# Performance work log

Hardware: AMD Instinct MI355X
Metric: run time of the kernel (lower is better)

Reference implementation:

```python
import jax, jax.numpy as jnp
import numpy as np

B, H, W, C = 64, 32, 32, 256
HZ, WZ = 16, 16
N = 64          # hidden_dim = n_proposals
K = 3           # dynamic depthwise kernel size
EPS = 1e-5


def _layernorm(x, g, b):
    mu = jnp.mean(x, axis=-1, keepdims=True)
    var = jnp.var(x, axis=-1, keepdims=True)
    return (x - mu) * jax.lax.rsqrt(var + EPS) * g + b


def setup_inputs() -> dict:
    key = jax.random.key(0)
    ks = jax.random.split(key, 8)
    s = 0.02  # weight init scale
    return {
        "x_feat": jax.random.normal(ks[0], (B, H, W, C), jnp.float32),
        "z_feat": jax.random.normal(ks[1], (B, HZ, WZ, C), jnp.float32),
        "Wz": jax.random.normal(ks[2], (C, N), jnp.float32) * s,
        "bz": jnp.zeros((N,), jnp.float32),
        "Wx": jax.random.normal(ks[3], (C, N), jnp.float32) * s,
        "bx": jnp.zeros((N,), jnp.float32),
        "Wdyn": jax.random.normal(ks[4], (C, N + K), jnp.float32) * s,
        "bdyn": jnp.zeros((N + K,), jnp.float32),
        "g_norm": jnp.ones((C,), jnp.float32),
        "b_norm": jnp.zeros((C,), jnp.float32),
        "Wp": jax.random.normal(ks[5], (C, 1), jnp.float32) * s,
        "bp": jnp.zeros((1,), jnp.float32),
        "g_ln": jnp.ones((C,), jnp.float32),
        "b_ln": jnp.zeros((C,), jnp.float32),
    }


def _dysep_conv_atten(query, value, Wdyn, bdyn, g_norm, b_norm):
    # query, value: [B, N, C]
    dy = query @ Wdyn + bdyn                      # [B, N, N+K]
    w_depth = dy[:, :, :K]                        # [B, N, K] per-channel depthwise kernels
    w_point = dy[:, :, K:]                        # [B, N, N] per-sample pointwise (1x1) weights
    # depthwise conv along C with 'same' padding (torch conv1d = cross-correlation)
    vpad = jnp.pad(value, ((0, 0), (0, 0), (1, 1)))
    depth = (w_depth[..., 0:1] * vpad[:, :, 0:C]
             + w_depth[..., 1:2] * vpad[:, :, 1:C + 1]
             + w_depth[..., 2:3] * vpad[:, :, 2:C + 2])
    depth = jax.nn.relu(depth)                    # [B, N, C]
    point = jnp.einsum('bnm,bmc->bnc', w_point, depth)
    return _layernorm(point, g_norm, b_norm)


def reference(x_feat, z_feat, Wz, bz, Wx, bx, Wdyn, bdyn,
              g_norm, b_norm, Wp, bp, g_ln, b_ln):
    # kernels from template features (detached in the original: kernels.detach())
    z_core = z_feat @ Wz + bz                                   # [B,HZ,WZ,N]
    kernels = jnp.einsum('bhwn,bhwc->bnc', z_core, z_feat)      # [B,N,C]
    kernels = jax.lax.stop_gradient(kernels)

    x_n = x_feat @ Wx + bx                                      # [B,H,W,N]
    kernels_x = jnp.einsum('bhwn,bhwc->bnc', x_n, x_feat)       # [B,N,C]
    kernels_x = _dysep_conv_atten(kernels, kernels_x, Wdyn, bdyn, g_norm, b_norm)

    x_corr = jnp.einsum('bnc,bhwn->bhwc', kernels_x, x_n)       # [B,H,W,C]
    proto = kernels_x @ Wp + bp                                 # [B,N,1]
    tem = jax.nn.sigmoid(jnp.einsum('bnd,bnc->bdc', proto, kernels_x))  # [B,1,C]
    tem = tem[:, :, None, :]                                    # [B,1,1,C]
    x_corr = x_corr * tem

    return x_feat + jax.nn.relu(_layernorm(x_corr, g_ln, b_ln))
```

## Files before the change

kernel.cpp:

```cpp
#include <hip/hip_runtime.h>
#include <math.h>

#define EPSV 1e-5f

typedef __attribute__((ext_vector_type(8))) short short8;
typedef __attribute__((ext_vector_type(4))) float f32x4;

static __device__ __forceinline__ unsigned bfpack2(float lo, float hi) {
    union { float f; unsigned u; } a, b;
    a.f = lo; b.f = hi;
    unsigned ua = a.u + 0x7fffu + ((a.u >> 16) & 1u);
    unsigned ub = b.u + 0x7fffu + ((b.u >> 16) & 1u);
    return (ua >> 16) | (ub & 0xffff0000u);
}

__global__ __launch_bounds__(256) void gemm_all(
    const float* __restrict__ Xx, const float* __restrict__ Wxp,
    const float* __restrict__ bxp, float* __restrict__ Yx,
    const float* __restrict__ Xz, const float* __restrict__ Wzp,
    const float* __restrict__ bzp,
    unsigned short* __restrict__ xnbT, unsigned short* __restrict__ xfbT,
    unsigned short* __restrict__ zcbT, unsigned short* __restrict__ zfbT)
{
    __shared__ float Xc[16 * 132];
    __shared__ float Wc[16 * 64];
    const int t = threadIdx.x;
    const float *X, *W, *bias; float* Y;
    unsigned short *Tn, *Tf;
    long r0; int P, bb, p0;
    if (blockIdx.x < 512) {
        X = Xx; W = Wxp; bias = bxp; Y = Yx;
        r0 = (long)blockIdx.x * 128;
        P = 1024; bb = blockIdx.x >> 3; p0 = (blockIdx.x & 7) * 128;
        Tn = xnbT; Tf = xfbT;
    } else {
        int zb = blockIdx.x - 512;
        X = Xz; W = Wzp; bias = bzp; Y = nullptr;
        r0 = (long)zb * 128;
        P = 256; bb = zb >> 1; p0 = (zb & 1) * 128;
        Tn = zcbT; Tf = zfbT;
    }

    const int tr = t >> 4, tc = t & 15;
    float4 bv = *(const float4*)(bias + tc * 4);
    float acc[8][4];
#pragma unroll
    for (int i = 0; i < 8; ++i) { acc[i][0]=bv.x; acc[i][1]=bv.y; acc[i][2]=bv.z; acc[i][3]=bv.w; }

    const int lr = t >> 2;
    const int lc = (t & 3) * 4;
    const int wl = t >> 4, wj = (t & 15) * 4;
    float4 xv0 = *(const float4*)(X + (r0 + lr) * 256 + lc);
    float4 xv1 = *(const float4*)(X + (r0 + lr + 64) * 256 + lc);
    float4 wv  = *(const float4*)(W + (long)wl * 64 + wj);

    for (int c0 = 0; c0 < 256; c0 += 16) {
        Xc[(lc+0)*132 + lr] = xv0.x; Xc[(lc+1)*132 + lr] = xv0.y;
        Xc[(lc+2)*132 + lr] = xv0.z; Xc[(lc+3)*132 + lr] = xv0.w;
        Xc[(lc+0)*132 + lr+64] = xv1.x; Xc[(lc+1)*132 + lr+64] = xv1.y;
        Xc[(lc+2)*132 + lr+64] = xv1.z; Xc[(lc+3)*132 + lr+64] = xv1.w;
        *(float4*)&Wc[wl * 64 + wj] = wv;
        __syncthreads();
        if (c0 + 16 < 256) {
            xv0 = *(const float4*)(X + (r0 + lr) * 256 + c0 + 16 + lc);
            xv1 = *(const float4*)(X + (r0 + lr + 64) * 256 + c0 + 16 + lc);
            wv  = *(const float4*)(W + (long)(c0 + 16 + wl) * 64 + wj);
        }
#pragma unroll
        for (int cl = 0; cl < 16; ++cl) {
            float4 a0 = *(float4*)&Xc[cl * 132 + tr * 8];
            float4 a1 = *(float4*)&Xc[cl * 132 + tr * 8 + 4];
            float4 b4 = *(float4*)&Wc[cl * 64 + tc * 4];
            acc[0][0]+=a0.x*b4.x; acc[0][1]+=a0.x*b4.y; acc[0][2]+=a0.x*b4.z; acc[0][3]+=a0.x*b4.w;
            acc[1][0]+=a0.y*b4.x; acc[1][1]+=a0.y*b4.y; acc[1][2]+=a0.y*b4.z; acc[1][3]+=a0.y*b4.w;
            acc[2][0]+=a0.z*b4.x; acc[2][1]+=a0.z*b4.y; acc[2][2]+=a0.z*b4.z; acc[2][3]+=a0.z*b4.w;
            acc[3][0]+=a0.w*b4.x; acc[3][1]+=a0.w*b4.y; acc[3][2]+=a0.w*b4.z; acc[3][3]+=a0.w*b4.w;
            acc[4][0]+=a1.x*b4.x; acc[4][1]+=a1.x*b4.y; acc[4][2]+=a1.x*b4.z; acc[4][3]+=a1.x*b4.w;
            acc[5][0]+=a1.y*b4.x; acc[5][1]+=a1.y*b4.y; acc[5][2]+=a1.y*b4.z; acc[5][3]+=a1.y*b4.w;
            acc[6][0]+=a1.z*b4.x; acc[6][1]+=a1.z*b4.y; acc[6][2]+=a1.z*b4.z; acc[6][3]+=a1.z*b4.w;
            acc[7][0]+=a1.w*b4.x; acc[7][1]+=a1.w*b4.y; acc[7][2]+=a1.w*b4.z; acc[7][3]+=a1.w*b4.w;
        }
        {
            int cl2 = t >> 4, p8 = (t & 15) * 8;
            const float* xr = &Xc[cl2 * 132 + p8];
            uint4 pk;
            pk.x = bfpack2(xr[0], xr[1]); pk.y = bfpack2(xr[2], xr[3]);
            pk.z = bfpack2(xr[4], xr[5]); pk.w = bfpack2(xr[6], xr[7]);
            *(uint4*)(Tf + ((long)(bb * 256 + c0 + cl2)) * P + p0 + p8) = pk;
        }
        __syncthreads();
    }
    if (Y) {
#pragma unroll
        for (int i = 0; i < 8; ++i) {
            float4 o = make_float4(acc[i][0], acc[i][1], acc[i][2], acc[i][3]);
            *(float4*)(Y + (r0 + tr * 8 + i) * 64 + tc * 4) = o;
        }
    }
#pragma unroll
    for (int j = 0; j < 4; ++j) {
        int n = tc * 4 + j;
        uint4 pk;
        pk.x = bfpack2(acc[0][j], acc[1][j]);
        pk.y = bfpack2(acc[2][j], acc[3][j]);
        pk.z = bfpack2(acc[4][j], acc[5][j]);
        pk.w = bfpack2(acc[6][j], acc[7][j]);
        *(uint4*)(Tn + ((long)(bb * 64 + n)) * P + p0 + tr * 8) = pk;
    }
}

__global__ __launch_bounds__(256) void corr_mfma(
    const unsigned short* __restrict__ xnbT, const unsigned short* __restrict__ xfbT,
    float* __restrict__ kxr,
    const unsigned short* __restrict__ zcbT, const unsigned short* __restrict__ zfbT,
    float* __restrict__ kern)
{
    __shared__ __align__(16) unsigned short AT[64 * 136];
    __shared__ __align__(16) unsigned short BT[64 * 136];
    const int t = threadIdx.x;
    const unsigned short *Ab, *Bb; float* S; int b, P;
    if (blockIdx.y < 64) { b = blockIdx.y;      Ab = xnbT; Bb = xfbT; S = kxr;  P = 1024; }
    else                 { b = blockIdx.y - 64; Ab = zcbT; Bb = zfbT; S = kern; P = 256;  }
    const int ct = blockIdx.x;
    const int w = t >> 6, l = t & 63;
    const int quad = l >> 4, lane16 = l & 15;

    const unsigned short* Abase = Ab + (long)b * 64 * P;
    const unsigned short* Bbase = Bb + ((long)(b * 256 + ct * 64)) * P;
    const int srow = t >> 4, sk = (t & 15) * 8;

    f32x4 acc[4] = {{0.f,0.f,0.f,0.f},{0.f,0.f,0.f,0.f},{0.f,0.f,0.f,0.f},{0.f,0.f,0.f,0.f}};

    uint4 pa[4], pb[4];
#pragma unroll
    for (int i = 0; i < 4; ++i) {
        int row = srow + i * 16;
        pa[i] = *(const uint4*)(Abase + (long)row * P + sk);
        pb[i] = *(const uint4*)(Bbase + (long)row * P + sk);
    }
    const int nk = P >> 7;
    for (int kc = 0; kc < nk; ++kc) {
#pragma unroll
        for (int i = 0; i < 4; ++i) {
            int row = srow + i * 16;
            *(uint4*)&AT[row * 136 + sk] = pa[i];
            *(uint4*)&BT[row * 136 + sk] = pb[i];
        }
        __syncthreads();
        if (kc + 1 < nk) {
            int ko = (kc + 1) * 128 + sk;
#pragma unroll
            for (int i = 0; i < 4; ++i) {
                int row = srow + i * 16;
                pa[i] = *(const uint4*)(Abase + (long)row * P + ko);
                pb[i] = *(const uint4*)(Bbase + (long)row * P + ko);
            }
        }
#pragma unroll
        for (int ks = 0; ks < 4; ++ks) {
            const int ko2 = ks * 32 + quad * 8;
            short8 bfrag = *(const short8*)&BT[(w * 16 + lane16) * 136 + ko2];
#pragma unroll
            for (int mi = 0; mi < 4; ++mi) {
                short8 afrag = *(const short8*)&AT[(mi * 16 + lane16) * 136 + ko2];
                acc[mi] = __builtin_amdgcn_mfma_f32_16x16x32_bf16(afrag, bfrag, acc[mi], 0, 0, 0);
            }
        }
        __syncthreads();
    }
#pragma unroll
    for (int mi = 0; mi < 4; ++mi) {
        long row = (long)(b * 64 + mi * 16 + quad * 4);
        int col = ct * 64 + w * 16 + lane16;
#pragma unroll
        for (int r = 0; r < 4; ++r)
            S[(row + r) * 256 + col] = acc[mi][r];
    }
}

__global__ __launch_bounds__(256) void dy_all(
    const float* __restrict__ kern, const float* __restrict__ Wdyn,
    const float* __restrict__ bdyn, float* __restrict__ dyb)
{
    __shared__ float Ac[16 * 64];
    __shared__ float Wc[16 * 64];
    __shared__ float Wd3[48];
    const int b = blockIdx.x, t = threadIdx.x;
    const int tr = t >> 4, tc = t & 15;
    float acc[4][4];
#pragma unroll
    for (int j = 0; j < 4; ++j) {
        float bj = bdyn[3 + tc * 4 + j];
        acc[0][j] = bj; acc[1][j] = bj; acc[2][j] = bj; acc[3][j] = bj;
    }
    const int lr = t >> 2, lc = (t & 3) * 4;
    const int wl = t >> 4, wj = (t & 15) * 4;
    const int nwd = t / 3, jwd = t - nwd * 3;
    float wdacc = 0.f;
    float4 av = *(const float4*)(kern + ((long)(b * 64 + lr)) * 256 + lc);
    float w0 = Wdyn[wl * 67 + 3 + wj + 0];
    float w1 = Wdyn[wl * 67 + 3 + wj + 1];
    float w2 = Wdyn[wl * 67 + 3 + wj + 2];
    float w3 = Wdyn[wl * 67 + 3 + wj + 3];
    float wdr = (t < 48) ? Wdyn[(t / 3) * 67 + (t % 3)] : 0.f;

    for (int c0 = 0; c0 < 256; c0 += 16) {
        Ac[(lc+0)*64 + lr] = av.x; Ac[(lc+1)*64 + lr] = av.y;
        Ac[(lc+2)*64 + lr] = av.z; Ac[(lc+3)*64 + lr] = av.w;
        Wc[wl*64 + wj+0] = w0; Wc[wl*64 + wj+1] = w1;
        Wc[wl*64 + wj+2] = w2; Wc[wl*64 + wj+3] = w3;
        if (t < 48) Wd3[t] = wdr;
        __syncthreads();
        if (c0 + 16 < 256) {
            av = *(const float4*)(kern + ((long)(b * 64 + lr)) * 256 + c0 + 16 + lc);
            w0 = Wdyn[(c0 + 16 + wl) * 67 + 3 + wj + 0];
            w1 = Wdyn[(c0 + 16 + wl) * 67 + 3 + wj + 1];
            w2 = Wdyn[(c0 + 16 + wl) * 67 + 3 + wj + 2];
            w3 = Wdyn[(c0 + 16 + wl) * 67 + 3 + wj + 3];
            if (t < 48) wdr = Wdyn[(c0 + 16 + t / 3) * 67 + (t % 3)];
        }
#pragma unroll
        for (int cl = 0; cl < 16; ++cl) {
            float4 a = *(float4*)&Ac[cl * 64 + tr * 4];
            float4 w = *(float4*)&Wc[cl * 64 + tc * 4];
            acc[0][0]+=a.x*w.x; acc[0][1]+=a.x*w.y; acc[0][2]+=a.x*w.z; acc[0][3]+=a.x*w.w;
            acc[1][0]+=a.y*w.x; acc[1][1]+=a.y*w.y; acc[1][2]+=a.y*w.z; acc[1][3]+=a.y*w.w;
            acc[2][0]+=a.z*w.x; acc[2][1]+=a.z*w.y; acc[2][2]+=a.z*w.z; acc[2][3]+=a.z*w.w;
            acc[3][0]+=a.w*w.x; acc[3][1]+=a.w*w.y; acc[3][2]+=a.w*w.z; acc[3][3]+=a.w*w.w;
        }
        if (t < 192) {
#pragma unroll
            for (int cl = 0; cl < 16; ++cl)
                wdacc += Ac[cl * 64 + nwd] * Wd3[cl * 3 + jwd];
        }
        __syncthreads();
    }
#pragma unroll
    for (int i = 0; i < 4; ++i) {
        float4 o = make_float4(acc[i][0], acc[i][1], acc[i][2], acc[i][3]);
        *(float4*)(dyb + ((long)(b * 64 + tr * 4 + i)) * 68 + tc * 4) = o;
    }
    if (t < 192) dyb[((long)(b * 64 + nwd)) * 68 + 64 + jwd] = wdacc + bdyn[jwd];
}

__global__ __launch_bounds__(256) void depthpoint(
    const float* __restrict__ dyb, const float* __restrict__ v,
    const float* __restrict__ g, const float* __restrict__ Wp,
    float* __restrict__ point, float* __restrict__ partials)
{
    __shared__ float smem[13312];
    float* wpT = smem;
    float* wd3 = smem + 4352;
    float* vt  = smem + 4608;
    float* dep = smem + 8960;
    float* rs  = vt;

    const int t = threadIdx.x;
    const int b = blockIdx.y, ct = blockIdx.x, c0 = ct * 64;
    const int tr = t >> 4, tc = t & 15;

#pragma unroll
    for (int i = 0; i < 4; ++i) {
        int idx = t + i * 256; int n = idx >> 4, m0 = (idx & 15) * 4;
        float4 w4 = *(const float4*)(dyb + ((long)(b * 64 + n)) * 68 + m0);
        wpT[(m0+0)*68 + n] = w4.x; wpT[(m0+1)*68 + n] = w4.y;
        wpT[(m0+2)*68 + n] = w4.z; wpT[(m0+3)*68 + n] = w4.w;
    }
    if (t < 64) {
        long o = ((long)(b * 64 + t)) * 68 + 64;
        wd3[t*4+0] = dyb[o+0]; wd3[t*4+1] = dyb[o+1]; wd3[t*4+2] = dyb[o+2];
    }
    {
        int m = t >> 2, lc0 = (t & 3) * 17;
#pragma unroll
        for (int k = 0; k < 17; ++k) {
            int lc = lc0 + k;
            if (lc < 66) {
                int c = c0 - 1 + lc;
                vt[m * 68 + lc] = (c >= 0 && c < 256) ? v[((long)(b * 64 + m)) * 256 + c] : 0.f;
            }
        }
    }
    __syncthreads();
#pragma unroll
    for (int im = 0; im < 4; ++im) {
        int m = tr * 4 + im;
        float w0 = wd3[m*4+0], w1 = wd3[m*4+1], w2 = wd3[m*4+2];
#pragma unroll
        for (int jc = 0; jc < 4; ++jc) {
            int cl = tc * 4 + jc;
            float d = w0 * vt[m*68 + cl] + w1 * vt[m*68 + cl + 1] + w2 * vt[m*68 + cl + 2];
            dep[m*68 + cl] = fmaxf(d, 0.f);
        }
    }
    __syncthreads();
    float acc[4][4] = {};
#pragma unroll 16
    for (int m = 0; m < 64; ++m) {
        float4 a4 = *(float4*)&wpT[m * 68 + tr * 4];
        float4 d4 = *(float4*)&dep[m * 68 + tc * 4];
        acc[0][0]+=a4.x*d4.x; acc[0][1]+=a4.x*d4.y; acc[0][2]+=a4.x*d4.z; acc[0][3]+=a4.x*d4.w;
        acc[1][0]+=a4.y*d4.x; acc[1][1]+=a4.y*d4.y; acc[1][2]+=a4.y*d4.z; acc[1][3]+=a4.y*d4.w;
        acc[2][0]+=a4.z*d4.x; acc[2][1]+=a4.z*d4.y; acc[2][2]+=a4.z*d4.z; acc[2][3]+=a4.z*d4.w;
        acc[3][0]+=a4.w*d4.x; acc[3][1]+=a4.w*d4.y; acc[3][2]+=a4.w*d4.z; acc[3][3]+=a4.w*d4.w;
    }
    int cg = c0 + tc * 4;
    float4 g4  = *(const float4*)(g + cg);
    float4 wp4 = *(const float4*)(Wp + cg);
    float gw0 = g4.x*wp4.x, gw1 = g4.y*wp4.y, gw2 = g4.z*wp4.z, gw3 = g4.w*wp4.w;
#pragma unroll
    for (int i = 0; i < 4; ++i) {
        float4 o = make_float4(acc[i][0], acc[i][1], acc[i][2], acc[i][3]);
        *(float4*)(point + ((long)(b * 64 + tr * 4 + i)) * 256 + cg) = o;
        float s  = o.x + o.y + o.z + o.w;
        float s2 = o.x*o.x + o.y*o.y + o.z*o.z + o.w*o.w;
        float dg = o.x*gw0 + o.y*gw1 + o.z*gw2 + o.w*gw3;
        rs[0*1088 + (tr*4+i)*17 + tc] = s;
        rs[1*1088 + (tr*4+i)*17 + tc] = s2;
        rs[2*1088 + (tr*4+i)*17 + tc] = dg;
    }
    __syncthreads();
    if (t < 64) {
        float s = 0.f, s2 = 0.f, dg = 0.f;
#pragma unroll
        for (int j = 0; j < 16; ++j) {
            s  += rs[t*17 + j];
            s2 += rs[1088 + t*17 + j];
            dg += rs[2176 + t*17 + j];
        }
        long base = ((long)(b * 4 + ct)) * 192;
        partials[base + t]        = s;
        partials[base + 64 + t]   = s2;
        partials[base + 128 + t]  = dg;
    }
}

__global__ __launch_bounds__(256) void lntem(
    const float* __restrict__ partials, const float* __restrict__ point,
    const float* __restrict__ g, const float* __restrict__ bta,
    const float* __restrict__ Wp, const float* __restrict__ bp,
    float* __restrict__ murr, float* __restrict__ AB)
{
    __shared__ float sA[256], sB[256];
    __shared__ float wnv[64];
    __shared__ float tot[4];
    const int b = blockIdx.x, t = threadIdx.x;
    const int c = t;
    float gc = g[c], bc = bta[c], wpc = Wp[c];
    sA[t] = gc * wpc; sB[t] = bc * wpc;
    __syncthreads();
    for (int off = 128; off >= 1; off >>= 1) {
        if (t < off) { sA[t] += sA[t+off]; sB[t] += sB[t+off]; }
        __syncthreads();
    }
    if (t == 0) { tot[0] = sA[0]; tot[1] = sB[0] + bp[0]; }
    __syncthreads();
    float Sgw = tot[0], Sbw = tot[1];

    float protoe = 0.f, mu = 0.f, rr = 0.f;
    if (t < 64) {
        float S1 = 0.f, S2 = 0.f, Sdg = 0.f;
#pragma unroll
        for (int ct = 0; ct < 4; ++ct) {
            long o = ((long)(b * 4 + ct)) * 192;
            S1 += partials[o + t]; S2 += partials[o + 64 + t]; Sdg += partials[o + 128 + t];
        }
        mu = S1 * (1.f / 256.f);
        float var = S2 * (1.f / 256.f) - mu * mu;
        rr = rsqrtf(var + EPSV);
        protoe = rr * (Sdg - mu * Sgw) + Sbw;
        wnv[t] = protoe * rr;
        murr[b * 128 + 2*t]     = rr;
        murr[b * 128 + 2*t + 1] = -mu * rr;
    }
    __syncthreads();
    sA[t] = (t < 64) ? protoe * rr * mu : 0.f;
    sB[t] = (t < 64) ? protoe : 0.f;
    __syncthreads();
    for (int off = 128; off >= 1; off >>= 1) {
        if (t < off) { sA[t] += sA[t+off]; sB[t] += sB[t+off]; }
        __syncthreads();
    }
    if (t == 0) { tot[2] = sA[0]; tot[3] = sB[0]; }
    __syncthreads();
    float Bv = tot[2], Sv = tot[3];

    const float* pcol = point + (long)b * 64 * 256 + c;
    float a0 = 0.f, a1 = 0.f, a2 = 0.f, a3 = 0.f;
#pragma unroll
    for (int n = 0; n < 64; n += 4) {
        a0 += wnv[n+0] * pcol[(n+0) * 256];
        a1 += wnv[n+1] * pcol[(n+1) * 256];
        a2 += wnv[n+2] * pcol[(n+2) * 256];
        a3 += wnv[n+3] * pcol[(n+3) * 256];
    }
    float accA = a0 + a1 + a2 + a3;
    float x = gc * (accA - Bv) + bc * Sv;
    float temv = 1.f / (1.f + expf(-x));
    AB[b * 512 + c]       = gc * temv;
    AB[b * 512 + 256 + c] = bc * temv;
}

__global__ __launch_bounds__(256) void final_kernel(
    const float* __restrict__ xn, const float* __restrict__ point,
    const float* __restrict__ murr, const float* __restrict__ AB,
    const float* __restrict__ xf, const float* __restrict__ g,
    const float* __restrict__ bt, float* __restrict__ out)
{
    __shared__ float xtT[64 * 68];
    __shared__ float kc[64 * 68];
    __shared__ float rs1[64 * 17], rs2[64 * 17];
    __shared__ float mu[64], rr[64];
    __shared__ float rq[128];
    const int t = threadIdx.x;
    const int b = blockIdx.y;
    const int pg = blockIdx.x;
    const int tr = t >> 4;
    const int tc = t & 15;

    if (t < 128) rq[t] = murr[b * 128 + t];
    {
        int row = t >> 2, q = t & 3;
        const float* src = xn + ((long)(b * 1024 + pg * 64 + row)) * 64 + q * 16;
        float4 f0 = *(const float4*)(src + 0);
        float4 f1 = *(const float4*)(src + 4);
        float4 f2 = *(const float4*)(src + 8);
        float4 f3 = *(const float4*)(src + 12);
        int n0 = q * 16;
        xtT[(n0+ 0)*68+row]=f0.x; xtT[(n0+ 1)*68+row]=f0.y; xtT[(n0+ 2)*68+row]=f0.z; xtT[(n0+ 3)*68+row]=f0.w;
        xtT[(n0+ 4)*68+row]=f1.x; xtT[(n0+ 5)*68+row]=f1.y; xtT[(n0+ 6)*68+row]=f1.z; xtT[(n0+ 7)*68+row]=f1.w;
        xtT[(n0+ 8)*68+row]=f2.x; xtT[(n0+ 9)*68+row]=f2.y; xtT[(n0+10)*68+row]=f2.z; xtT[(n0+11)*68+row]=f2.w;
        xtT[(n0+12)*68+row]=f3.x; xtT[(n0+13)*68+row]=f3.y; xtT[(n0+14)*68+row]=f3.z; xtT[(n0+15)*68+row]=f3.w;
    }

    float4 xcv[4][4];
    float si[4] = {0.f,0.f,0.f,0.f}, s2i[4] = {0.f,0.f,0.f,0.f};
#pragma unroll
    for (int cc = 0; cc < 4; ++cc) {
        __syncthreads();
#pragma unroll
        for (int i = 0; i < 4; ++i) {
            int idx = t + i * 256;
            int n = idx >> 4, jq = idx & 15;
            int cb = cc * 64 + jq * 4;
            float4 p4 = *(const float4*)(point + ((long)(b * 64 + n)) * 256 + cb);
            float rn = rq[2*n], qn = rq[2*n + 1];
            float4 A4 = *(const float4*)(AB + b * 512 + cb);
            float4 B4 = *(const float4*)(AB + b * 512 + 256 + cb);
            float4 kv;
            kv.x = (p4.x * rn + qn) * A4.x + B4.x;
            kv.y = (p4.y * rn + qn) * A4.y + B4.y;
            kv.z = (p4.z * rn + qn) * A4.z + B4.z;
            kv.w = (p4.w * rn + qn) * A4.w + B4.w;
            *(float4*)&kc[n * 68 + jq * 4] = kv;
        }
        __syncthreads();
        float4 a0 = {0,0,0,0}, a1 = {0,0,0,0}, a2 = {0,0,0,0}, a3 = {0,0,0,0};
#pragma unroll 8
        for (int n = 0; n < 64; ++n) {
            float4 xv = *(float4*)&xtT[n * 68 + tr * 4];
            float4 kv = *(float4*)&kc[n * 68 + tc * 4];
            a0.x += xv.x*kv.x; a0.y += xv.x*kv.y; a0.z += xv.x*kv.z; a0.w += xv.x*kv.w;
            a1.x += xv.y*kv.x; a1.y += xv.y*kv.y; a1.z += xv.y*kv.z; a1.w += xv.y*kv.w;
            a2.x += xv.z*kv.x; a2.y += xv.z*kv.y; a2.z += xv.z*kv.z; a2.w += xv.z*kv.w;
            a3.x += xv.w*kv.x; a3.y += xv.w*kv.y; a3.z += xv.w*kv.z; a3.w += xv.w*kv.w;
        }
        xcv[cc][0] = a0; xcv[cc][1] = a1; xcv[cc][2] = a2; xcv[cc][3] = a3;
        si[0] += a0.x+a0.y+a0.z+a0.w;  s2i[0] += a0.x*a0.x+a0.y*a0.y+a0.z*a0.z+a0.w*a0.w;
        si[1] += a1.x+a1.y+a1.z+a1.w;  s2i[1] += a1.x*a1.x+a1.y*a1.y+a1.z*a1.z+a1.w*a1.w;
        si[2] += a2.x+a2.y+a2.z+a2.w;  s2i[2] += a2.x*a2.x+a2.y*a2.y+a2.z*a2.z+a2.w*a2.w;
        si[3] += a3.x+a3.y+a3.z+a3.w;  s2i[3] += a3.x*a3.x+a3.y*a3.y+a3.z*a3.z+a3.w*a3.w;
    }
#pragma unroll
    for (int i = 0; i < 4; ++i) { rs1[(tr*4+i)*17 + tc] = si[i]; rs2[(tr*4+i)*17 + tc] = s2i[i]; }
    __syncthreads();
    if (t < 64) {
        float s = 0.f, s2 = 0.f;
#pragma unroll
        for (int k = 0; k < 16; ++k) { s += rs1[t*17 + k]; s2 += rs2[t*17 + k]; }
        float m = s * (1.f / 256.f);
        mu[t] = m; rr[t] = rsqrtf(s2 * (1.f / 256.f) - m * m + EPSV);
    }
    __syncthreads();
#pragma unroll
    for (int cc = 0; cc < 4; ++cc) {
        int cb = cc * 64 + tc * 4;
        float4 g4 = *(const float4*)(g + cb);
        float4 b4 = *(const float4*)(bt + cb);
#pragma unroll
        for (int i = 0; i < 4; ++i) {
            int row = tr * 4 + i;
            float m = mu[row], r = rr[row];
            long grow = ((long)(b * 1024 + pg * 64 + row)) * 256;
            float4 xfv = *(const float4*)(xf + grow + cb);
            float4 a = xcv[cc][i];
            float4 o;
            o.x = xfv.x + fmaxf((a.x - m) * r * g4.x + b4.x, 0.f);
            o.y = xfv.y + fmaxf((a.y - m) * r * g4.y + b4.y, 0.f);
            o.z = xfv.z + fmaxf((a.z - m) * r * g4.z + b4.z, 0.f);
            o.w = xfv.w + fmaxf((a.w - m) * r * g4.w + b4.w, 0.f);
            *(float4*)(out + grow + cb) = o;
        }
    }
}

extern "C" void kernel_launch(void* const* d_in, const int* in_sizes, int n_in,
                              void* d_out, int out_size, void* d_ws, size_t ws_size,
                              hipStream_t stream)
{
    (void)in_sizes; (void)n_in; (void)out_size; (void)ws_size;
    const float* x_feat = (const float*)d_in[0];
    const float* z_feat = (const float*)d_in[1];
    const float* Wz     = (const float*)d_in[2];
    const float* bz     = (const float*)d_in[3];
    const float* Wx     = (const float*)d_in[4];
    const float* bx     = (const float*)d_in[5];
    const float* Wdyn   = (const float*)d_in[6];
    const float* bdyn   = (const float*)d_in[7];
    const float* g_norm = (const float*)d_in[8];
    const float* b_norm = (const float*)d_in[9];
    const float* Wp     = (const float*)d_in[10];
    const float* bp     = (const float*)d_in[11];
    const float* g_ln   = (const float*)d_in[12];
    const float* b_ln   = (const float*)d_in[13];
    float* out = (float*)d_out;

    float* ws       = (float*)d_ws;
    float* xn       = ws;
    float* kern     = xn + 4194304;
    float* kxr      = kern + 1048576;
    float* point    = kxr + 1048576;
    float* dyb      = point + 1048576;
    float* partials = dyb + 278528;
    float* murr     = partials + 49152;
    float* AB       = murr + 8192;
    unsigned short* xnbT = (unsigned short*)(AB + 32768);
    unsigned short* xfbT = xnbT + 4194304;
    unsigned short* zcbT = xfbT + 16777216;
    unsigned short* zfbT = zcbT + 1048576;

    gemm_all<<<640, 256, 0, stream>>>(x_feat, Wx, bx, xn, z_feat, Wz, bz,
                                      xnbT, xfbT, zcbT, zfbT);
    corr_mfma<<<dim3(4, 128), 256, 0, stream>>>(xnbT, xfbT, kxr, zcbT, zfbT, kern);
    dy_all<<<64, 256, 0, stream>>>(kern, Wdyn, bdyn, dyb);
    depthpoint<<<dim3(4, 64), 256, 0, stream>>>(dyb, kxr, g_norm, Wp, point, partials);
    lntem<<<64, 256, 0, stream>>>(partials, point, g_norm, b_norm, Wp, bp, murr, AB);
    final_kernel<<<dim3(16, 64), 256, 0, stream>>>(xn, point, murr, AB, x_feat, g_ln, b_ln, out);
}
```

Before: 285.8 us.

## Reassociate projections via per-batch Gram matrices and fold Wx into final GEMM

Replaces the x/z projection GEMM plus correlation with a per-batch Gram matrix X^T X (bf16 MFMA) followed by a small projection by W, with bias handled through column sums. The final stage no longer reads the projected x_n. Instead it builds a per-batch 256x256 matrix M = kernels_x^T-scaled times Wx and runs an MFMA GEMM straight from x_feat, with LayerNorm fused in. This avoids writing and reading the large transposed bf16 copies of x_feat and x_n. In exchange it does more FLOPs on the Gram matrices and reads x_feat with strided column loads, and the reassociation changes bf16 rounding.

```diff
diff --git a/kernel.cpp b/kernel.cpp
--- a/kernel.cpp
+++ b/kernel.cpp
@@ -14,167 +14,155 @@
     return (ua >> 16) | (ub & 0xffff0000u);
 }
 
-__global__ __launch_bounds__(256) void gemm_all(
-    const float* __restrict__ Xx, const float* __restrict__ Wxp,
-    const float* __restrict__ bxp, float* __restrict__ Yx,
-    const float* __restrict__ Xz, const float* __restrict__ Wzp,
-    const float* __restrict__ bzp,
-    unsigned short* __restrict__ xnbT, unsigned short* __restrict__ xfbT,
-    unsigned short* __restrict__ zcbT, unsigned short* __restrict__ zfbT)
-{
-    __shared__ float Xc[16 * 132];
-    __shared__ float Wc[16 * 64];
+__global__ __launch_bounds__(256) void gram(
+    const float* __restrict__ Xx, const float* __restrict__ Xz,
+    float* __restrict__ Gx, float* __restrict__ Gz,
+    float* __restrict__ csx, float* __restrict__ csz)
+{
+    __shared__ __align__(16) unsigned short AT[64 * 72];
+    __shared__ __align__(16) unsigned short BT[64 * 72];
+    __shared__ float csr[256];
+    int id = blockIdx.x;
+    const float* X; float* G; float* cs; int P;
+    if (id < 1024) { X = Xx; G = Gx; cs = csx; P = 1024; }
+    else { id -= 1024; X = Xz; G = Gz; cs = csz; P = 256; }
+    const int b = id & 63;
+    const int tile = id >> 6;
+    const int ci = tile >> 2, cj = tile & 3;
+    const int nk = P >> 6;
     const int t = threadIdx.x;
-    const float *X, *W, *bias; float* Y;
-    unsigned short *Tn, *Tf;
-    long r0; int P, bb, p0;
-    if (blockIdx.x < 512) {
-        X = Xx; W = Wxp; bias = bxp; Y = Yx;
-        r0 = (long)blockIdx.x * 128;
-        P = 1024; bb = blockIdx.x >> 3; p0 = (blockIdx.x & 7) * 128;
-        Tn = xnbT; Tf = xfbT;
-    } else {
-        int zb = blockIdx.x - 512;
-        X = Xz; W = Wzp; bias = bzp; Y = nullptr;
-        r0 = (long)zb * 128;
-        P = 256; bb = zb >> 1; p0 = (zb & 1) * 128;
-        Tn = zcbT; Tf = zfbT;
-    }
-
-    const int tr = t >> 4, tc = t & 15;
-    float4 bv = *(const float4*)(bias + tc * 4);
-    float acc[8][4];
-#pragma unroll
-    for (int i = 0; i < 8; ++i) { acc[i][0]=bv.x; acc[i][1]=bv.y; acc[i][2]=bv.z; acc[i][3]=bv.w; }
-
-    const int lr = t >> 2;
-    const int lc = (t & 3) * 4;
-    const int wl = t >> 4, wj = (t & 15) * 4;
-    float4 xv0 = *(const float4*)(X + (r0 + lr) * 256 + lc);
-    float4 xv1 = *(const float4*)(X + (r0 + lr + 64) * 256 + lc);
-    float4 wv  = *(const float4*)(W + (long)wl * 64 + wj);
-
-    for (int c0 = 0; c0 < 256; c0 += 16) {
-        Xc[(lc+0)*132 + lr] = xv0.x; Xc[(lc+1)*132 + lr] = xv0.y;
-        Xc[(lc+2)*132 + lr] = xv0.z; Xc[(lc+3)*132 + lr] = xv0.w;
-        Xc[(lc+0)*132 + lr+64] = xv1.x; Xc[(lc+1)*132 + lr+64] = xv1.y;
-        Xc[(lc+2)*132 + lr+64] = xv1.z; Xc[(lc+3)*132 + lr+64] = xv1.w;
-        *(float4*)&Wc[wl * 64 + wj] = wv;
-        __syncthreads();
-        if (c0 + 16 < 256) {
-            xv0 = *(const float4*)(X + (r0 + lr) * 256 + c0 + 16 + lc);
-            xv1 = *(const float4*)(X + (r0 + lr + 64) * 256 + c0 + 16 + lc);
-            wv  = *(const float4*)(W + (long)(c0 + 16 + wl) * 64 + wj);
-        }
-#pragma unroll
-        for (int cl = 0; cl < 16; ++cl) {
-            float4 a0 = *(float4*)&Xc[cl * 132 + tr * 8];
-            float4 a1 = *(float4*)&Xc[cl * 132 + tr * 8 + 4];
-            float4 b4 = *(float4*)&Wc[cl * 64 + tc * 4];
-            acc[0][0]+=a0.x*b4.x; acc[0][1]+=a0.x*b4.y; acc[0][2]+=a0.x*b4.z; acc[0][3]+=a0.x*b4.w;
-            acc[1][0]+=a0.y*b4.x; acc[1][1]+=a0.y*b4.y; acc[1][2]+=a0.y*b4.z; acc[1][3]+=a0.y*b4.w;
-            acc[2][0]+=a0.z*b4.x; acc[2][1]+=a0.z*b4.y; acc[2][2]+=a0.z*b4.z; acc[2][3]+=a0.z*b4.w;
-            acc[3][0]+=a0.w*b4.x; acc[3][1]+=a0.w*b4.y; acc[3][2]+=a0.w*b4.z; acc[3][3]+=a0.w*b4.w;
-            acc[4][0]+=a1.x*b4.x; acc[4][1]+=a1.x*b4.y; acc[4][2]+=a1.x*b4.z; acc[4][3]+=a1.x*b4.w;
-            acc[5][0]+=a1.y*b4.x; acc[5][1]+=a1.y*b4.y; acc[5][2]+=a1.y*b4.z; acc[5][3]+=a1.y*b4.w;
-            acc[6][0]+=a1.z*b4.x; acc[6][1]+=a1.z*b4.y; acc[6][2]+=a1.z*b4.z; acc[6][3]+=a1.z*b4.w;
-            acc[7][0]+=a1.w*b4.x; acc[7][1]+=a1.w*b4.y; acc[7][2]+=a1.w*b4.z; acc[7][3]+=a1.w*b4.w;
-        }
-        {
-            int cl2 = t >> 4, p8 = (t & 15) * 8;
-            const float* xr = &Xc[cl2 * 132 + p8];
-            uint4 pk;
-            pk.x = bfpack2(xr[0], xr[1]); pk.y = bfpack2(xr[2], xr[3]);
-            pk.z = bfpack2(xr[4], xr[5]); pk.w = bfpack2(xr[6], xr[7]);
-            *(uint4*)(Tf + ((long)(bb * 256 + c0 + cl2)) * P + p0 + p8) = pk;
-        }
-        __syncthreads();
-    }
-    if (Y) {
-#pragma unroll
-        for (int i = 0; i < 8; ++i) {
-            float4 o = make_float4(acc[i][0], acc[i][1], acc[i][2], acc[i][3]);
-            *(float4*)(Y + (r0 + tr * 8 + i) * 64 + tc * 4) = o;
-        }
-    }
-#pragma unroll
-    for (int j = 0; j < 4; ++j) {
-        int n = tc * 4 + j;
-        uint4 pk;
-        pk.x = bfpack2(acc[0][j], acc[1][j]);
-        pk.y = bfpack2(acc[2][j], acc[3][j]);
-        pk.z = bfpack2(acc[4][j], acc[5][j]);
-        pk.w = bfpack2(acc[6][j], acc[7][j]);
-        *(uint4*)(Tn + ((long)(bb * 64 + n)) * P + p0 + tr * 8) = pk;
-    }
-}
-
-__global__ __launch_bounds__(256) void corr_mfma(
-    const unsigned short* __restrict__ xnbT, const unsigned short* __restrict__ xfbT,
+    const int cl = t & 63, ph = t >> 6;
+    const int w = t >> 6, quad = (t >> 4) & 3, lane16 = t & 15;
+    const float* Xb = X + (long)b * P * 256;
+    const float* Acol = Xb + ci * 64 + cl;
+    const float* Bcol = Xb + cj * 64 + cl;
+    const bool diag = (ci == cj);
+
+    f32x4 acc[4] = {{0.f,0.f,0.f,0.f},{0.f,0.f,0.f,0.f},{0.f,0.f,0.f,0.f},{0.f,0.f,0.f,0.f}};
+    float csum = 0.f;
+
+    for (int kc = 0; kc < nk; ++kc) {
+        const int p0 = kc * 64 + ph * 16;
+        float va[16], vb[16];
+#pragma unroll
+        for (int k = 0; k < 16; ++k) va[k] = Acol[(long)(p0 + k) * 256];
+        if (!diag) {
+#pragma unroll
+            for (int k = 0; k < 16; ++k) vb[k] = Bcol[(long)(p0 + k) * 256];
+        } else {
+#pragma unroll
+            for (int k = 0; k < 16; ++k) { vb[k] = va[k]; csum += va[k]; }
+        }
+        uint4 a0, a1, b0, b1;
+        a0.x = bfpack2(va[0], va[1]);   a0.y = bfpack2(va[2], va[3]);
+        a0.z = bfpack2(va[4], va[5]);   a0.w = bfpack2(va[6], va[7]);
+        a1.x = bfpack2(va[8], va[9]);   a1.y = bfpack2(va[10], va[11]);
+        a1.z = bfpack2(va[12], va[13]); a1.w = bfpack2(va[14], va[15]);
+        b0.x = bfpack2(vb[0], vb[1]);   b0.y = bfpack2(vb[2], vb[3]);
+        b0.z = bfpack2(vb[4], vb[5]);   b0.w = bfpack2(vb[6], vb[7]);
+        b1.x = bfpack2(vb[8], vb[9]);   b1.y = bfpack2(vb[10], vb[11]);
+        b1.z = bfpack2(vb[12], vb[13]); b1.w = bfpack2(vb[14], vb[15]);
+        __syncthreads();
+        *(uint4*)&AT[cl * 72 + ph * 16]     = a0;
+        *(uint4*)&AT[cl * 72 + ph * 16 + 8] = a1;
+        *(uint4*)&BT[cl * 72 + ph * 16]     = b0;
+        *(uint4*)&BT[cl * 72 + ph * 16 + 8] = b1;
+        __syncthreads();
+#pragma unroll
+        for (int ks = 0; ks < 2; ++ks) {
+            const int ko = ks * 32 + quad * 8;
+            short8 bfrag = *(const short8*)&BT[(w * 16 + lane16) * 72 + ko];
+#pragma unroll
+            for (int mi = 0; mi < 4; ++mi) {
+                short8 afrag = *(const short8*)&AT[(mi * 16 + lane16) * 72 + ko];
+                acc[mi] = __builtin_amdgcn_mfma_f32_16x16x32_bf16(afrag, bfrag, acc[mi], 0, 0, 0);
+            }
+        }
+    }
+#pragma unroll
+    for (int mi = 0; mi < 4; ++mi) {
+        long row = (long)(b * 256 + ci * 64 + mi * 16 + quad * 4);
+        int col = cj * 64 + w * 16 + lane16;
+#pragma unroll
+        for (int r = 0; r < 4; ++r)
+            G[(row + r) * 256 + col] = acc[mi][r];
+    }
+    if (diag) {
+        csr[ph * 64 + cl] = csum;
+        __syncthreads();
+        if (t < 64)
+            cs[b * 256 + ci * 64 + t] = csr[t] + csr[64 + t] + csr[128 + t] + csr[192 + t];
+    }
+}
+
+__global__ __launch_bounds__(256) void proj(
+    const float* __restrict__ Gx, const float* __restrict__ csx,
+    const float* __restrict__ Wx, const float* __restrict__ bx,
     float* __restrict__ kxr,
-    const unsigned short* __restrict__ zcbT, const unsigned short* __restrict__ zfbT,
+    const float* __restrict__ Gz, const float* __restrict__ csz,
+    const float* __restrict__ Wz, const float* __restrict__ bz,
     float* __restrict__ kern)
 {
-    __shared__ __align__(16) unsigned short AT[64 * 136];
-    __shared__ __align__(16) unsigned short BT[64 * 136];
+    __shared__ __align__(16) unsigned short ATW[64 * 264];
+    __shared__ __align__(16) unsigned short BTC[64 * 72];
     const int t = threadIdx.x;
-    const unsigned short *Ab, *Bb; float* S; int b, P;
-    if (blockIdx.y < 64) { b = blockIdx.y;      Ab = xnbT; Bb = xfbT; S = kxr;  P = 1024; }
-    else                 { b = blockIdx.y - 64; Ab = zcbT; Bb = zfbT; S = kern; P = 256;  }
-    const int ct = blockIdx.x;
-    const int w = t >> 6, l = t & 63;
-    const int quad = l >> 4, lane16 = l & 15;
-
-    const unsigned short* Abase = Ab + (long)b * 64 * P;
-    const unsigned short* Bbase = Bb + ((long)(b * 256 + ct * 64)) * P;
-    const int srow = t >> 4, sk = (t & 15) * 8;
-
+    const int id = blockIdx.x;
+    const int b = id & 63, s = id >> 6;
+    const float *G, *cs, *W, *bias; float* O;
+    if (s < 4) { G = Gx; cs = csx; W = Wx; bias = bx; O = kxr; }
+    else       { G = Gz; cs = csz; W = Wz; bias = bz; O = kern; }
+    const int ct = s & 3;
+    const int n = t & 63, ph = t >> 6;
+#pragma unroll
+    for (int cc = 0; cc < 4; ++cc) {
+        float v[16];
+#pragma unroll
+        for (int k = 0; k < 16; ++k) v[k] = W[(ph * 64 + cc * 16 + k) * 64 + n];
+        uint4 p0, p1;
+        p0.x = bfpack2(v[0], v[1]);   p0.y = bfpack2(v[2], v[3]);
+        p0.z = bfpack2(v[4], v[5]);   p0.w = bfpack2(v[6], v[7]);
+        p1.x = bfpack2(v[8], v[9]);   p1.y = bfpack2(v[10], v[11]);
+        p1.z = bfpack2(v[12], v[13]); p1.w = bfpack2(v[14], v[15]);
+        *(uint4*)&ATW[n * 264 + ph * 64 + cc * 16]     = p0;
+        *(uint4*)&ATW[n * 264 + ph * 64 + cc * 16 + 8] = p1;
+    }
+    const int row = t >> 2, cq = t & 3;
+    const int w = t >> 6, quad = (t >> 4) & 3, lane16 = t & 15;
+    const float* Grow = G + ((long)(b * 256 + ct * 64 + row)) * 256 + cq * 16;
     f32x4 acc[4] = {{0.f,0.f,0.f,0.f},{0.f,0.f,0.f,0.f},{0.f,0.f,0.f,0.f},{0.f,0.f,0.f,0.f}};
-
-    uint4 pa[4], pb[4];
-#pragma unroll
-    for (int i = 0; i < 4; ++i) {
-        int row = srow + i * 16;
-        pa[i] = *(const uint4*)(Abase + (long)row * P + sk);
-        pb[i] = *(const uint4*)(Bbase + (long)row * P + sk);
-    }
-    const int nk = P >> 7;
-    for (int kc = 0; kc < nk; ++kc) {
-#pragma unroll
-        for (int i = 0; i < 4; ++i) {
-            int row = srow + i * 16;
-            *(uint4*)&AT[row * 136 + sk] = pa[i];
-            *(uint4*)&BT[row * 136 + sk] = pb[i];
-        }
-        __syncthreads();
-        if (kc + 1 < nk) {
-            int ko = (kc + 1) * 128 + sk;
-#pragma unroll
-            for (int i = 0; i < 4; ++i) {
-                int row = srow + i * 16;
-                pa[i] = *(const uint4*)(Abase + (long)row * P + ko);
-                pb[i] = *(const uint4*)(Bbase + (long)row * P + ko);
-            }
-        }
-#pragma unroll
-        for (int ks = 0; ks < 4; ++ks) {
-            const int ko2 = ks * 32 + quad * 8;
-            short8 bfrag = *(const short8*)&BT[(w * 16 + lane16) * 136 + ko2];
+    for (int kc = 0; kc < 4; ++kc) {
+        float4 g0 = *(const float4*)(Grow + kc * 64 + 0);
+        float4 g1 = *(const float4*)(Grow + kc * 64 + 4);
+        float4 g2 = *(const float4*)(Grow + kc * 64 + 8);
+        float4 g3 = *(const float4*)(Grow + kc * 64 + 12);
+        uint4 pk0, pk1;
+        pk0.x = bfpack2(g0.x, g0.y); pk0.y = bfpack2(g0.z, g0.w);
+        pk0.z = bfpack2(g1.x, g1.y); pk0.w = bfpack2(g1.z, g1.w);
+        pk1.x = bfpack2(g2.x, g2.y); pk1.y = bfpack2(g2.z, g2.w);
+        pk1.z = bfpack2(g3.x, g3.y); pk1.w = bfpack2(g3.z, g3.w);
+        __syncthreads();
+        *(uint4*)&BTC[row * 72 + cq * 16]     = pk0;
+        *(uint4*)&BTC[row * 72 + cq * 16 + 8] = pk1;
+        __syncthreads();
+#pragma unroll
+        for (int ks = 0; ks < 2; ++ks) {
+            const int ko = ks * 32 + quad * 8;
+            short8 bfrag = *(const short8*)&BTC[(w * 16 + lane16) * 72 + ko];
 #pragma unroll
             for (int mi = 0; mi < 4; ++mi) {
-                short8 afrag = *(const short8*)&AT[(mi * 16 + lane16) * 136 + ko2];
+                short8 afrag = *(const short8*)&ATW[(mi * 16 + lane16) * 264 + kc * 64 + ko];
                 acc[mi] = __builtin_amdgcn_mfma_f32_16x16x32_bf16(afrag, bfrag, acc[mi], 0, 0, 0);
             }
         }
-        __syncthreads();
-    }
+    }
+    const int col = ct * 64 + w * 16 + lane16;
+    const float csv = cs[b * 256 + col];
 #pragma unroll
     for (int mi = 0; mi < 4; ++mi) {
-        long row = (long)(b * 64 + mi * 16 + quad * 4);
-        int col = ct * 64 + w * 16 + lane16;
+        const int nrow = mi * 16 + quad * 4;
 #pragma unroll
         for (int r = 0; r < 4; ++r)
-            S[(row + r) * 256 + col] = acc[mi][r];
+            O[((long)(b * 64 + nrow + r)) * 256 + col] = acc[mi][r] + bias[nrow + r] * csv;
     }
 }
 
@@ -401,105 +389,184 @@
     AB[b * 512 + 256 + c] = bc * temv;
 }
 
-__global__ __launch_bounds__(256) void final_kernel(
-    const float* __restrict__ xn, const float* __restrict__ point,
-    const float* __restrict__ murr, const float* __restrict__ AB,
-    const float* __restrict__ xf, const float* __restrict__ g,
-    const float* __restrict__ bt, float* __restrict__ out)
-{
-    __shared__ float xtT[64 * 68];
-    __shared__ float kc[64 * 68];
-    __shared__ float rs1[64 * 17], rs2[64 * 17];
-    __shared__ float mu[64], rr[64];
-    __shared__ float rq[128];
+__global__ __launch_bounds__(256) void buildM(
+    const float* __restrict__ point, const float* __restrict__ murr,
+    const float* __restrict__ AB, const float* __restrict__ Wx,
+    const float* __restrict__ bx,
+    unsigned short* __restrict__ MT, float* __restrict__ svec)
+{
+    __shared__ float ks_s[64 * 68];
+    __shared__ float wt_s[64 * 68];
     const int t = threadIdx.x;
-    const int b = blockIdx.y;
-    const int pg = blockIdx.x;
-    const int tr = t >> 4;
-    const int tc = t & 15;
-
-    if (t < 128) rq[t] = murr[b * 128 + t];
+    const int id = blockIdx.x;
+    const int b = id & 63, mt = id >> 6;
     {
-        int row = t >> 2, q = t & 3;
-        const float* src = xn + ((long)(b * 1024 + pg * 64 + row)) * 64 + q * 16;
-        float4 f0 = *(const float4*)(src + 0);
-        float4 f1 = *(const float4*)(src + 4);
-        float4 f2 = *(const float4*)(src + 8);
-        float4 f3 = *(const float4*)(src + 12);
-        int n0 = q * 16;
-        xtT[(n0+ 0)*68+row]=f0.x; xtT[(n0+ 1)*68+row]=f0.y; xtT[(n0+ 2)*68+row]=f0.z; xtT[(n0+ 3)*68+row]=f0.w;
-        xtT[(n0+ 4)*68+row]=f1.x; xtT[(n0+ 5)*68+row]=f1.y; xtT[(n0+ 6)*68+row]=f1.z; xtT[(n0+ 7)*68+row]=f1.w;
-        xtT[(n0+ 8)*68+row]=f2.x; xtT[(n0+ 9)*68+row]=f2.y; xtT[(n0+10)*68+row]=f2.z; xtT[(n0+11)*68+row]=f2.w;
-        xtT[(n0+12)*68+row]=f3.x; xtT[(n0+13)*68+row]=f3.y; xtT[(n0+14)*68+row]=f3.z; xtT[(n0+15)*68+row]=f3.w;
-    }
-
-    float4 xcv[4][4];
-    float si[4] = {0.f,0.f,0.f,0.f}, s2i[4] = {0.f,0.f,0.f,0.f};
-#pragma unroll
-    for (int cc = 0; cc < 4; ++cc) {
-        __syncthreads();
-#pragma unroll
-        for (int i = 0; i < 4; ++i) {
-            int idx = t + i * 256;
-            int n = idx >> 4, jq = idx & 15;
-            int cb = cc * 64 + jq * 4;
-            float4 p4 = *(const float4*)(point + ((long)(b * 64 + n)) * 256 + cb);
-            float rn = rq[2*n], qn = rq[2*n + 1];
-            float4 A4 = *(const float4*)(AB + b * 512 + cb);
-            float4 B4 = *(const float4*)(AB + b * 512 + 256 + cb);
+        const int n = t >> 2, q = t & 3;
+        const float rn = murr[b * 128 + 2 * n], qn = murr[b * 128 + 2 * n + 1];
+        const float* prow = point + ((long)(b * 64 + n)) * 256 + mt * 64 + q * 16;
+        const float* Arow = AB + b * 512 + mt * 64 + q * 16;
+#pragma unroll
+        for (int j = 0; j < 4; ++j) {
+            float4 p4 = *(const float4*)(prow + j * 4);
+            float4 A4 = *(const float4*)(Arow + j * 4);
+            float4 B4 = *(const float4*)(Arow + 256 + j * 4);
             float4 kv;
             kv.x = (p4.x * rn + qn) * A4.x + B4.x;
             kv.y = (p4.y * rn + qn) * A4.y + B4.y;
             kv.z = (p4.z * rn + qn) * A4.z + B4.z;
             kv.w = (p4.w * rn + qn) * A4.w + B4.w;
-            *(float4*)&kc[n * 68 + jq * 4] = kv;
-        }
-        __syncthreads();
-        float4 a0 = {0,0,0,0}, a1 = {0,0,0,0}, a2 = {0,0,0,0}, a3 = {0,0,0,0};
-#pragma unroll 8
-        for (int n = 0; n < 64; ++n) {
-            float4 xv = *(float4*)&xtT[n * 68 + tr * 4];
-            float4 kv = *(float4*)&kc[n * 68 + tc * 4];
-            a0.x += xv.x*kv.x; a0.y += xv.x*kv.y; a0.z += xv.x*kv.z; a0.w += xv.x*kv.w;
-            a1.x += xv.y*kv.x; a1.y += xv.y*kv.y; a1.z += xv.y*kv.z; a1.w += xv.y*kv.w;
-            a2.x += xv.z*kv.x; a2.y += xv.z*kv.y; a2.z += xv.z*kv.z; a2.w += xv.z*kv.w;
-            a3.x += xv.w*kv.x; a3.y += xv.w*kv.y; a3.z += xv.w*kv.z; a3.w += xv.w*kv.w;
-        }
-        xcv[cc][0] = a0; xcv[cc][1] = a1; xcv[cc][2] = a2; xcv[cc][3] = a3;
-        si[0] += a0.x+a0.y+a0.z+a0.w;  s2i[0] += a0.x*a0.x+a0.y*a0.y+a0.z*a0.z+a0.w*a0.w;
-        si[1] += a1.x+a1.y+a1.z+a1.w;  s2i[1] += a1.x*a1.x+a1.y*a1.y+a1.z*a1.z+a1.w*a1.w;
-        si[2] += a2.x+a2.y+a2.z+a2.w;  s2i[2] += a2.x*a2.x+a2.y*a2.y+a2.z*a2.z+a2.w*a2.w;
-        si[3] += a3.x+a3.y+a3.z+a3.w;  s2i[3] += a3.x*a3.x+a3.y*a3.y+a3.z*a3.z+a3.w*a3.w;
-    }
-#pragma unroll
-    for (int i = 0; i < 4; ++i) { rs1[(tr*4+i)*17 + tc] = si[i]; rs2[(tr*4+i)*17 + tc] = s2i[i]; }
+            *(float4*)&ks_s[n * 68 + q * 16 + j * 4] = kv;
+        }
+    }
     __syncthreads();
     if (t < 64) {
-        float s = 0.f, s2 = 0.f;
-#pragma unroll
-        for (int k = 0; k < 16; ++k) { s += rs1[t*17 + k]; s2 += rs2[t*17 + k]; }
-        float m = s * (1.f / 256.f);
-        mu[t] = m; rr[t] = rsqrtf(s2 * (1.f / 256.f) - m * m + EPSV);
-    }
-    __syncthreads();
-#pragma unroll
+        float sv = 0.f;
+#pragma unroll
+        for (int n2 = 0; n2 < 64; ++n2) sv += bx[n2] * ks_s[n2 * 68 + t];
+        svec[b * 256 + mt * 64 + t] = sv;
+    }
+    const int tr = t >> 4, tc = t & 15;
+    const int nw = t & 63, ph = t >> 6;
     for (int cc = 0; cc < 4; ++cc) {
-        int cb = cc * 64 + tc * 4;
-        float4 g4 = *(const float4*)(g + cb);
-        float4 b4 = *(const float4*)(bt + cb);
+        float wv[16];
+#pragma unroll
+        for (int k = 0; k < 16; ++k) wv[k] = Wx[(cc * 64 + ph * 16 + k) * 64 + nw];
+        __syncthreads();
+#pragma unroll
+        for (int k = 0; k < 16; ++k) wt_s[nw * 68 + ph * 16 + k] = wv[k];
+        __syncthreads();
+        float a2[4][4] = {};
+#pragma unroll 16
+        for (int n2 = 0; n2 < 64; ++n2) {
+            float4 a4 = *(float4*)&ks_s[n2 * 68 + tr * 4];
+            float4 w4 = *(float4*)&wt_s[n2 * 68 + tc * 4];
+            a2[0][0]+=a4.x*w4.x; a2[0][1]+=a4.x*w4.y; a2[0][2]+=a4.x*w4.z; a2[0][3]+=a4.x*w4.w;
+            a2[1][0]+=a4.y*w4.x; a2[1][1]+=a4.y*w4.y; a2[1][2]+=a4.y*w4.z; a2[1][3]+=a4.y*w4.w;
+            a2[2][0]+=a4.z*w4.x; a2[2][1]+=a4.z*w4.y; a2[2][2]+=a4.z*w4.z; a2[2][3]+=a4.z*w4.w;
+            a2[3][0]+=a4.w*w4.x; a2[3][1]+=a4.w*w4.y; a2[3][2]+=a4.w*w4.z; a2[3][3]+=a4.w*w4.w;
+        }
 #pragma unroll
         for (int i = 0; i < 4; ++i) {
-            int row = tr * 4 + i;
-            float m = mu[row], r = rr[row];
-            long grow = ((long)(b * 1024 + pg * 64 + row)) * 256;
-            float4 xfv = *(const float4*)(xf + grow + cb);
-            float4 a = xcv[cc][i];
-            float4 o;
-            o.x = xfv.x + fmaxf((a.x - m) * r * g4.x + b4.x, 0.f);
-            o.y = xfv.y + fmaxf((a.y - m) * r * g4.y + b4.y, 0.f);
-            o.z = xfv.z + fmaxf((a.z - m) * r * g4.z + b4.z, 0.f);
-            o.w = xfv.w + fmaxf((a.w - m) * r * g4.w + b4.w, 0.f);
-            *(float4*)(out + grow + cb) = o;
+            uint2 pk;
+            pk.x = bfpack2(a2[i][0], a2[i][1]);
+            pk.y = bfpack2(a2[i][2], a2[i][3]);
+            *(uint2*)&MT[((long)(b * 256 + mt * 64 + tr * 4 + i)) * 256 + cc * 64 + tc * 4] = pk;
+        }
+    }
+}
+
+__global__ __launch_bounds__(256) void final2(
+    const float* __restrict__ xf, const unsigned short* __restrict__ MT,
+    const float* __restrict__ svec, const float* __restrict__ g,
+    const float* __restrict__ bt, float* __restrict__ out)
+{
+    __shared__ __align__(16) float SlArr[64 * 132];
+    __shared__ float red1[256], red2[256];
+    __shared__ float muS[64], rrS[64];
+    unsigned short* XT = (unsigned short*)SlArr;
+    float* Sl = SlArr;
+    const int t = threadIdx.x;
+    const int id = blockIdx.x;
+    const int b = id & 63, pt = id >> 6;
+    const int w = t >> 6, quad = (t >> 4) & 3, lane16 = t & 15;
+    const float* Xb = xf + ((long)(b * 1024 + pt * 64)) * 256;
+    {
+        const int p = t >> 2, q = t & 3;
+#pragma unroll
+        for (int j = 0; j < 4; ++j)
+#pragma unroll
+            for (int i = 0; i < 4; ++i) {
+                const int c = j * 64 + q * 16 + i * 4;
+                float4 v = *(const float4*)(Xb + (long)p * 256 + c);
+                uint2 pk;
+                pk.x = bfpack2(v.x, v.y);
+                pk.y = bfpack2(v.z, v.w);
+                *(uint2*)&XT[p * 264 + c] = pk;
+            }
+    }
+    __syncthreads();
+    f32x4 acc[4][4] = {};
+    const unsigned short* Mb = MT + (long)b * 65536;
+    for (int ks = 0; ks < 8; ++ks) {
+        const int ko = ks * 32 + quad * 8;
+        short8 bf4[4], af4[4];
+#pragma unroll
+        for (int ni = 0; ni < 4; ++ni)
+            bf4[ni] = *(const short8*)(Mb + (long)(w * 64 + ni * 16 + lane16) * 256 + ko);
+#pragma unroll
+        for (int mi = 0; mi < 4; ++mi)
+            af4[mi] = *(const short8*)&XT[(mi * 16 + lane16) * 264 + ko];
+#pragma unroll
+        for (int mi = 0; mi < 4; ++mi)
+#pragma unroll
+            for (int ni = 0; ni < 4; ++ni)
+                acc[mi][ni] = __builtin_amdgcn_mfma_f32_16x16x32_bf16(af4[mi], bf4[ni], acc[mi][ni], 0, 0, 0);
+    }
+    float sv4[4];
+#pragma unroll
+    for (int ni = 0; ni < 4; ++ni) sv4[ni] = svec[b * 256 + w * 64 + ni * 16 + lane16];
+#pragma unroll
+    for (int mi = 0; mi < 4; ++mi)
+#pragma unroll
+        for (int r = 0; r < 4; ++r) {
+            float s1 = 0.f, s2 = 0.f;
+#pragma unroll
+            for (int ni = 0; ni < 4; ++ni) {
+                float v = acc[mi][ni][r] + sv4[ni];
+                acc[mi][ni][r] = v;
+                s1 += v; s2 += v * v;
+            }
+#pragma unroll
+            for (int m = 1; m <= 8; m <<= 1) {
+                s1 += __shfl_xor(s1, m);
+                s2 += __shfl_xor(s2, m);
+            }
+            if (lane16 == 0) {
+                red1[(mi * 16 + quad * 4 + r) * 4 + w] = s1;
+                red2[(mi * 16 + quad * 4 + r) * 4 + w] = s2;
+            }
+        }
+    __syncthreads();
+    if (t < 64) {
+        float sa = red1[t*4] + red1[t*4+1] + red1[t*4+2] + red1[t*4+3];
+        float sb = red2[t*4] + red2[t*4+1] + red2[t*4+2] + red2[t*4+3];
+        float m = sa * (1.f / 256.f);
+        muS[t] = m;
+        rrS[t] = rsqrtf(sb * (1.f / 256.f) - m * m + EPSV);
+    }
+#pragma unroll
+    for (int h = 0; h < 2; ++h) {
+        __syncthreads();
+        if ((w >> 1) == h) {
+            const int chalf = (w & 1) * 64;
+#pragma unroll
+            for (int mi = 0; mi < 4; ++mi)
+#pragma unroll
+                for (int ni = 0; ni < 4; ++ni)
+#pragma unroll
+                    for (int r = 0; r < 4; ++r)
+                        Sl[(mi * 16 + quad * 4 + r) * 132 + chalf + ni * 16 + lane16] = acc[mi][ni][r];
+        }
+        __syncthreads();
+        {
+            const int p = t >> 2, q = t & 3;
+            const float m = muS[p], rr = rrS[p];
+            const long grow = ((long)(b * 1024 + pt * 64 + p)) * 256;
+#pragma unroll
+            for (int j = 0; j < 8; ++j) {
+                const int cl = q * 32 + j * 4;
+                const int c = h * 128 + cl;
+                float4 a  = *(float4*)&Sl[p * 132 + cl];
+                float4 g4 = *(const float4*)(g + c);
+                float4 b4 = *(const float4*)(bt + c);
+                float4 xv = *(const float4*)(xf + grow + c);
+                float4 o;
+                o.x = xv.x + fmaxf((a.x - m) * rr * g4.x + b4.x, 0.f);
+                o.y = xv.y + fmaxf((a.y - m) * rr * g4.y + b4.y, 0.f);
+                o.z = xv.z + fmaxf((a.z - m) * rr * g4.z + b4.z, 0.f);
+                o.w = xv.w + fmaxf((a.w - m) * rr * g4.w + b4.w, 0.f);
+                *(float4*)(out + grow + c) = o;
+            }
         }
     }
 }
@@ -526,24 +593,25 @@
     float* out = (float*)d_out;
 
     float* ws       = (float*)d_ws;
-    float* xn       = ws;
-    float* kern     = xn + 4194304;
+    float* Gx       = ws;
+    float* Gz       = Gx + 4194304;
+    float* kern     = Gz + 4194304;
     float* kxr      = kern + 1048576;
     float* point    = kxr + 1048576;
     float* dyb      = point + 1048576;
     float* partials = dyb + 278528;
     float* murr     = partials + 49152;
     float* AB       = murr + 8192;
-    unsigned short* xnbT = (unsigned short*)(AB + 32768);
-    unsigned short* xfbT = xnbT + 4194304;
-    unsigned short* zcbT = xfbT + 16777216;
-    unsigned short* zfbT = zcbT + 1048576;
-
-    gemm_all<<<640, 256, 0, stream>>>(x_feat, Wx, bx, xn, z_feat, Wz, bz,
-                                      xnbT, xfbT, zcbT, zfbT);
-    corr_mfma<<<dim3(4, 128), 256, 0, stream>>>(xnbT, xfbT, kxr, zcbT, zfbT, kern);
+    float* csx      = AB + 32768;
+    float* csz      = csx + 16384;
+    float* svec     = csz + 16384;
+    unsigned short* MT = (unsigned short*)(svec + 16384);
+
+    gram<<<2048, 256, 0, stream>>>(x_feat, z_feat, Gx, Gz, csx, csz);
+    proj<<<512, 256, 0, stream>>>(Gx, csx, Wx, bx, kxr, Gz, csz, Wz, bz, kern);
     dy_all<<<64, 256, 0, stream>>>(kern, Wdyn, bdyn, dyb);
     depthpoint<<<dim3(4, 64), 256, 0, stream>>>(dyb, kxr, g_norm, Wp, point, partials);
     lntem<<<64, 256, 0, stream>>>(partials, point, g_norm, b_norm, Wp, bp, murr, AB);
-    final_kernel<<<dim3(16, 64), 256, 0, stream>>>(xn, point, murr, AB, x_feat, g_ln, b_ln, out);
-}
+    buildM<<<256, 256, 0, stream>>>(point, murr, AB, Wx, bx, MT, svec);
+    final2<<<1024, 256, 0, stream>>>(x_feat, MT, svec, g_ln, b_ln, out);
+}
```

After: 299.2 us. 1.05x slower.
